# Optimization experiments

Hardware: AMD Instinct MI355X
Metric: run time of the kernel (lower is better)

The kernel has to match this reference:

```python
import jax, jax.numpy as jnp
import numpy as np

H = 12  # num_attention_heads


def setup_inputs() -> dict:
    key = jax.random.key(0)
    ks = jax.random.split(key, 7)
    B, T, L, D = 4, 64, 128, 768
    input_ids = jax.random.randint(ks[0], (B, T, L), 0, 30000, dtype=jnp.int32)
    speaker_ids = jax.random.randint(ks[1], (B, T), 0, 8, dtype=jnp.int32)
    token_embeddings = jax.random.normal(ks[2], (B, T, L, D), dtype=jnp.float32)
    edu_embeddings = jax.random.normal(ks[3], (B, T, D), dtype=jnp.float32)
    s = 1.0 / np.sqrt(D)
    Wk = jax.random.normal(ks[4], (D, D), dtype=jnp.float32) * s
    Wv = jax.random.normal(ks[5], (D, D), dtype=jnp.float32) * s
    Wq = jax.random.normal(ks[6], (D, D), dtype=jnp.float32) * s
    return {"input_ids": input_ids, "speaker_ids": speaker_ids,
            "token_embeddings": token_embeddings, "edu_embeddings": edu_embeddings,
            "Wk": Wk, "Wv": Wv, "Wq": Wq}


def reference(input_ids, speaker_ids, token_embeddings, edu_embeddings, Wk, Wv, Wq):
    B, T, L = input_ids.shape
    D = token_embeddings.shape[-1]
    d = D // H
    # per-turn keys/values, split into heads: [B,T,H,d]
    k = (edu_embeddings @ Wk.T).reshape(B, T, H, d)
    v = (edu_embeddings @ Wv.T).reshape(B, T, H, d)
    # per-head outer products k (x) v: [B,T,H,d,d]
    kv = jnp.einsum('bthd,bthe->bthde', k, v)
    # speaker-segmented inclusive prefix sum: M[b,t] = sum_{u<=t, spk[u]==spk[t]} kv[b,u]
    same = speaker_ids[:, None, :] == speaker_ids[:, :, None]        # [B,T(t),T(u)]
    causal = jnp.tril(jnp.ones((T, T), dtype=bool))                  # u <= t (inclusive)
    A = (same & causal).astype(kv.dtype)                             # [B,T,T]
    M = jnp.einsum('btu,buhde->bthde', A, kv)                        # [B,T,H,d,d]
    # token queries attend into their turn's speaker memory matrix
    q = (token_embeddings @ Wq.T).reshape(B, T, L, H, d)
    a = jnp.einsum('btlhd,bthde->btlhe', q, M).reshape(B, T, L, D)
    return token_embeddings + a
```

## Files before the change

kernel.cpp:

```cpp
#include <hip/hip_runtime.h>
#include <hip/hip_bf16.h>

#define NB 4
#define NT 64
#define NL 128
#define ND 768
#define NH 12
#define HD 64

typedef __attribute__((ext_vector_type(8))) short short8;
typedef __attribute__((ext_vector_type(4))) float f32x4;

typedef __attribute__((address_space(3))) unsigned int lds_u32;
typedef __attribute__((address_space(1))) const unsigned int glob_u32;

static __device__ __forceinline__ unsigned short f2b(float x) {
    __hip_bfloat16 h = __float2bfloat16(x);
    return *reinterpret_cast<unsigned short*>(&h);
}
static __device__ __forceinline__ void gl2lds16(const void* g, void* l) {
    __builtin_amdgcn_global_load_lds((glob_u32*)g, (lds_u32*)l, 16, 0, 0);
}
static __device__ __forceinline__ unsigned pkbf(float lo, float hi) {
    union { float f; unsigned u; } a, b; a.f = lo; b.f = hi;
    return __builtin_amdgcn_perm(b.u, a.u, 0x07060302u);
}

#define WQ_C   73728u
#define EDU_C  98304u
#define WK_C   172032u
#define NCHUNK 245760u

__global__ __launch_bounds__(256) void conv_bf16(
    const float* __restrict__ Wq, const float* __restrict__ edu,
    const float* __restrict__ Wk, const float* __restrict__ Wv,
    unsigned short* __restrict__ dst)
{
    size_t c = (size_t)blockIdx.x * 256 + threadIdx.x;
    if (c >= NCHUNK) return;
    const float* s;
    if (c < WQ_C)       s = Wq  + c * 8;
    else if (c < EDU_C) s = edu + (c - WQ_C)  * 8;
    else if (c < WK_C)  s = Wk  + (c - EDU_C) * 8;
    else                s = Wv  + (c - WK_C)  * 8;
    float4 x = *(const float4*)s;
    float4 y = *(const float4*)(s + 4);
    unsigned short v[8];
    v[0] = f2b(x.x); v[1] = f2b(x.y); v[2] = f2b(x.z); v[3] = f2b(x.w);
    v[4] = f2b(y.x); v[5] = f2b(y.y); v[6] = f2b(y.z); v[7] = f2b(y.w);
    *(short8*)(dst + c * 8) = *(short8*)v;
}

__global__ __launch_bounds__(256) void kvm(
    const unsigned short* __restrict__ edu_b,
    const unsigned short* __restrict__ wk_b,
    const unsigned short* __restrict__ wv_b,
    const int* __restrict__ spk,
    unsigned short* __restrict__ Mt)
{
    const int h = blockIdx.x, b = blockIdx.y, eh = blockIdx.z;

    __shared__ float bucket[8][32][65];
    __shared__ float k_s[64][68];
    __shared__ float v_s[64][36];
    __shared__ __align__(16) unsigned short stage[10240];
    __shared__ int spk_s[64];
    unsigned short* edu_s = stage;
    unsigned short* wk_s  = stage + 4096;
    unsigned short* wv_s  = stage + 8192;

    const int tid = threadIdx.x, lane = tid & 63, wvx = tid >> 6;
    const int lr = lane & 15, lg = lane >> 4, r8 = lane >> 3, l8 = lane & 7;

    { float* p = &bucket[0][0][0];
      for (int i = tid; i < 8 * 32 * 65; i += 256) p[i] = 0.f; }
    if (tid < 64) spk_s[tid] = spk[b * NT + tid];

    const unsigned short* edub = edu_b + (size_t)(b * 64) * ND;
    const unsigned short* wkb  = wk_b + (size_t)(h * 64) * ND;
    const unsigned short* wvb  = wv_b + (size_t)(h * 64 + eh * 32) * ND;

    f32x4 acc_k[4], acc_v[2];
    #pragma unroll
    for (int i = 0; i < 4; i++) acc_k[i] = (f32x4){0.f, 0.f, 0.f, 0.f};
    #pragma unroll
    for (int i = 0; i < 2; i++) acc_v[i] = (f32x4){0.f, 0.f, 0.f, 0.f};

    const int sswz = ((l8 ^ r8) * 8);

    for (int k0 = 0; k0 < ND; k0 += 64) {
        __syncthreads();
        #pragma unroll
        for (int j = 0; j < 5; j++) {
            const int cid = wvx * 5 + j;
            const unsigned short* gs; unsigned short* ls;
            if (cid < 8)       { gs = edub + (size_t)(cid * 8 + r8) * ND;        ls = edu_s + cid * 512; }
            else if (cid < 16) { gs = wkb  + (size_t)((cid - 8) * 8 + r8) * ND;  ls = wk_s + (cid - 8) * 512; }
            else               { gs = wvb  + (size_t)((cid - 16) * 8 + r8) * ND; ls = wv_s + (cid - 16) * 512; }
            gl2lds16(gs + k0 + sswz, ls);
        }
        __syncthreads();
        #pragma unroll
        for (int k32 = 0; k32 < 2; k32++) {
            const int cx = (((k32 * 4 + lg) ^ (lr & 7)) * 8);
            short8 eb = *(const short8*)&edu_s[(wvx * 16 + lr) * 64 + cx];
            #pragma unroll
            for (int jb = 0; jb < 4; jb++) {
                short8 ak = *(const short8*)&wk_s[(jb * 16 + lr) * 64 + cx];
                acc_k[jb] = __builtin_amdgcn_mfma_f32_16x16x32_bf16(ak, eb, acc_k[jb], 0, 0, 0);
            }
            #pragma unroll
            for (int jb = 0; jb < 2; jb++) {
                short8 av = *(const short8*)&wv_s[(jb * 16 + lr) * 64 + cx];
                acc_v[jb] = __builtin_amdgcn_mfma_f32_16x16x32_bf16(av, eb, acc_v[jb], 0, 0, 0);
            }
        }
    }

    {
        const int t = wvx * 16 + lr;
        #pragma unroll
        for (int jb = 0; jb < 4; jb++) *(f32x4*)&k_s[t][jb * 16 + lg * 4] = acc_k[jb];
        #pragma unroll
        for (int jb = 0; jb < 2; jb++) *(f32x4*)&v_s[t][jb * 16 + lg * 4] = acc_v[jb];
    }
    __syncthreads();

    const int e = tid & 31, dg = tid >> 5;
    for (int t = 0; t < NT; t++) {
        const int s = spk_s[t];
        const float vv = v_s[t][e];
        unsigned short tmp[8];
        #pragma unroll
        for (int jj = 0; jj < 8; jj++) {
            float m = bucket[s][e][dg * 8 + jj] + k_s[t][dg * 8 + jj] * vv;
            bucket[s][e][dg * 8 + jj] = m;
            tmp[jj] = f2b(m);
        }
        unsigned short* mpp = Mt + (((size_t)(b * NT + t) * NH + h) * HD + eh * 32 + e) * HD + dg * 8;
        *(short8*)mpp = *(short8*)tmp;
    }
}

__global__ __launch_bounds__(256, 2) void fused_qm(
    const float* __restrict__ te,
    const unsigned short* __restrict__ wq_b,
    const unsigned short* __restrict__ Mt,
    float* __restrict__ out)
{
    const int orig = blockIdx.x;
    const int id   = (orig & 7) * 192 + (orig >> 3);
    const int hp   = id % 6;
    const int bt   = id / 6;

    __shared__ __align__(16) unsigned short smem[32768];
    unsigned short* wq_s = smem;
    float*          te_s = (float*)(smem + 8192);
    unsigned short* mt_s = smem + 24576;
    unsigned short* q_s  = smem;

    const int tid  = threadIdx.x;
    const int lane = tid & 63;
    const int wvx  = tid >> 6;
    const int lr   = lane & 15;
    const int lg   = lane >> 4;
    const int wm   = wvx >> 1;
    const int wn   = wvx & 1;
    const int r8   = lane >> 3;
    const int l8   = lane & 7;

    const float*          teb = te + (size_t)bt * NL * ND;
    const unsigned short* wqb = wq_b + (size_t)hp * 128 * ND;

    {
        const unsigned short* mp = Mt + ((size_t)bt * NH + hp * 2) * (HD * HD);
        #pragma unroll
        for (int j = 0; j < 4; j++) {
            const int off = wvx * 2048 + j * 512;
            gl2lds16(mp + off + r8 * 64 + (l8 ^ r8) * 8, mt_s + off);
        }
    }

    f32x4 acc[4][4];
    #pragma unroll
    for (int i = 0; i < 4; i++)
        #pragma unroll
        for (int j = 0; j < 4; j++) acc[i][j] = (f32x4){0.f, 0.f, 0.f, 0.f};

    for (int k0 = 0; k0 < ND; k0 += 64) {
        __syncthreads();
        #pragma unroll
        for (int j = 0; j < 4; j++) {
            const int rbase = wvx * 32 + j * 8;
            gl2lds16(wqb + (size_t)(rbase + r8) * ND + k0 + (l8 ^ r8) * 8,
                     wq_s + rbase * 64);
        }
        #pragma unroll
        for (int j = 0; j < 8; j++) {
            const int rbase = wvx * 32 + j * 4;
            const int row   = rbase + (lane >> 4);
            const int c     = (lane & 15) ^ (row & 15);
            gl2lds16(teb + (size_t)row * ND + k0 + c * 4, te_s + rbase * 64);
        }
        __syncthreads();
        #pragma unroll
        for (int k32 = 0; k32 < 2; k32++) {
            short8 af[4], bf[4];
            #pragma unroll
            for (int tm = 0; tm < 4; tm++) {
                const int row = wm * 64 + tm * 16 + lr;
                af[tm] = *(const short8*)&wq_s[row * 64 + (((k32 * 4 + lg) ^ (lr & 7)) * 8)];
            }
            #pragma unroll
            for (int tn = 0; tn < 4; tn++) {
                const int row = wn * 64 + tn * 16 + lr;
                const int cg  = k32 * 8 + lg * 2;
                f32x4 x = *(const f32x4*)&te_s[row * 64 + ((cg ^ lr) * 4)];
                f32x4 y = *(const f32x4*)&te_s[row * 64 + (((cg + 1) ^ lr) * 4)];
                union { short8 s; unsigned u[4]; } bb;
                bb.u[0] = pkbf(x.x, x.y);
                bb.u[1] = pkbf(x.z, x.w);
                bb.u[2] = pkbf(y.x, y.y);
                bb.u[3] = pkbf(y.z, y.w);
                bf[tn] = bb.s;
            }
            #pragma unroll
            for (int tm = 0; tm < 4; tm++)
                #pragma unroll
                for (int tn = 0; tn < 4; tn++)
                    acc[tm][tn] = __builtin_amdgcn_mfma_f32_16x16x32_bf16(
                        af[tm], bf[tn], acc[tm][tn], 0, 0, 0);
        }
    }

    __syncthreads();

    #pragma unroll
    for (int tm = 0; tm < 4; tm++) {
        const int d0 = wm * 64 + tm * 16 + lg * 4;
        #pragma unroll
        for (int tn = 0; tn < 4; tn++) {
            const int ltok = wn * 64 + tn * 16 + lr;
            f32x4 a = acc[tm][tn];
            uint2 w2;
            w2.x = pkbf(a.x, a.y);
            w2.y = pkbf(a.z, a.w);
            *(uint2*)&q_s[ltok * 136 + d0] = w2;
        }
    }
    __syncthreads();

    const int h2 = wvx & 1;
    const int lh = wvx >> 1;
    f32x4 acc2[4][4];
    #pragma unroll
    for (int i = 0; i < 4; i++)
        #pragma unroll
        for (int j = 0; j < 4; j++) acc2[i][j] = (f32x4){0.f, 0.f, 0.f, 0.f};

    #pragma unroll
    for (int k32 = 0; k32 < 2; k32++) {
        const int ko = k32 * 32 + lg * 8;
        short8 af[4], bf[4];
        #pragma unroll
        for (int tm = 0; tm < 4; tm++)
            af[tm] = *(const short8*)&q_s[(lh * 64 + tm * 16 + lr) * 136 + h2 * 64 + ko];
        #pragma unroll
        for (int tn = 0; tn < 4; tn++) {
            const int row = h2 * 64 + tn * 16 + lr;
            bf[tn] = *(const short8*)&mt_s[row * 64 + (((k32 * 4 + lg) ^ (lr & 7)) * 8)];
        }
        #pragma unroll
        for (int tm = 0; tm < 4; tm++)
            #pragma unroll
            for (int tn = 0; tn < 4; tn++)
                acc2[tm][tn] = __builtin_amdgcn_mfma_f32_16x16x32_bf16(
                    af[tm], bf[tn], acc2[tm][tn], 0, 0, 0);
    }

    float* ob = out + (size_t)bt * NL * ND;
    #pragma unroll
    for (int tm = 0; tm < 4; tm++) {
        const int l0 = lh * 64 + tm * 16 + lg * 4;
        #pragma unroll
        for (int tn = 0; tn < 4; tn++) {
            const int cg = hp * 128 + h2 * 64 + tn * 16 + lr;
            f32x4 a = acc2[tm][tn];
            #pragma unroll
            for (int r = 0; r < 4; r++) {
                size_t gi = (size_t)(l0 + r) * ND + cg;
                ob[gi] = teb[gi] + a[r];
            }
        }
    }
}

extern "C" void kernel_launch(void* const* d_in, const int* in_sizes, int n_in,
                              void* d_out, int out_size, void* d_ws, size_t ws_size,
                              hipStream_t stream)
{
    const int*   spk = (const int*)d_in[1];
    const float* te  = (const float*)d_in[2];
    const float* edu = (const float*)d_in[3];
    const float* Wk  = (const float*)d_in[4];
    const float* Wv  = (const float*)d_in[5];
    const float* Wq  = (const float*)d_in[6];
    float* out = (float*)d_out;

    unsigned short* bf    = (unsigned short*)d_ws;
    unsigned short* wq_bb = bf;
    unsigned short* edu_b = bf + 589824u;
    unsigned short* wk_bb = bf + 786432u;
    unsigned short* wv_bb = bf + 1376256u;
    unsigned short* Mtbuf = bf + 1966080u;

    conv_bf16<<<960,             256, 0, stream>>>(Wq, edu, Wk, Wv, bf);
    kvm      <<<dim3(NH, NB, 2), 256, 0, stream>>>(edu_b, wk_bb, wv_bb, spk, Mtbuf);
    fused_qm <<<6 * NT * NB,     256, 0, stream>>>(te, wq_bb, Mtbuf, out);
}
```

Measured before the change: 109.9 us.

## Double-buffer Wq tiles, convert token embeddings to bf16 via registers, load M directly

Restructures the fused Q·M kernel's K loop. Token-embedding tiles are now prefetched into registers, converted to bf16, and written to LDS as bf16, and Wq tiles are double-buffered so the next tile's loads overlap the current tile's MFMAs. This shrinks LDS from 64KB to 48KB, which lets the launch bound ask for 3 blocks per CU. The M matrix is read straight from global into registers instead of being staged in LDS, and MFMA sections get raised wave priority. The cost is more register pressure, which at the higher occupancy target may cause spills, plus an extra barrier per half-iteration.

```diff
diff --git a/kernel.cpp b/kernel.cpp
--- a/kernel.cpp
+++ b/kernel.cpp
@@ -20,10 +20,6 @@
 }
 static __device__ __forceinline__ void gl2lds16(const void* g, void* l) {
     __builtin_amdgcn_global_load_lds((glob_u32*)g, (lds_u32*)l, 16, 0, 0);
-}
-static __device__ __forceinline__ unsigned pkbf(float lo, float hi) {
-    union { float f; unsigned u; } a, b; a.f = lo; b.f = hi;
-    return __builtin_amdgcn_perm(b.u, a.u, 0x07060302u);
 }
 
 #define WQ_C   73728u
@@ -142,7 +138,7 @@
     }
 }
 
-__global__ __launch_bounds__(256, 2) void fused_qm(
+__global__ __launch_bounds__(256, 3) void fused_qm(
     const float* __restrict__ te,
     const unsigned short* __restrict__ wq_b,
     const unsigned short* __restrict__ Mt,
@@ -153,10 +149,10 @@
     const int hp   = id % 6;
     const int bt   = id / 6;
 
-    __shared__ __align__(16) unsigned short smem[32768];
-    unsigned short* wq_s = smem;
-    float*          te_s = (float*)(smem + 8192);
-    unsigned short* mt_s = smem + 24576;
+    __shared__ __align__(16) unsigned short smem[24576];
+    unsigned short* te_s = smem;
+    unsigned short* wq0  = smem + 8192;
+    unsigned short* wq1  = smem + 16384;
     unsigned short* q_s  = smem;
 
     const int tid  = threadIdx.x;
@@ -168,72 +164,90 @@
     const int wn   = wvx & 1;
     const int r8   = lane >> 3;
     const int l8   = lane & 7;
+    const int sswz = (l8 ^ r8) * 8;
+    const int srow = tid >> 3;
+    const int sc   = tid & 7;
 
     const float*          teb = te + (size_t)bt * NL * ND;
     const unsigned short* wqb = wq_b + (size_t)hp * 128 * ND;
 
-    {
-        const unsigned short* mp = Mt + ((size_t)bt * NH + hp * 2) * (HD * HD);
-        #pragma unroll
-        for (int j = 0; j < 4; j++) {
-            const int off = wvx * 2048 + j * 512;
-            gl2lds16(mp + off + r8 * 64 + (l8 ^ r8) * 8, mt_s + off);
-        }
-    }
-
     f32x4 acc[4][4];
     #pragma unroll
     for (int i = 0; i < 4; i++)
         #pragma unroll
         for (int j = 0; j < 4; j++) acc[i][j] = (f32x4){0.f, 0.f, 0.f, 0.f};
 
-    for (int k0 = 0; k0 < ND; k0 += 64) {
-        __syncthreads();
+    float4 ld[4][2];
+
+    auto LOADREG = [&](int k0) {
+        #pragma unroll
+        for (int p = 0; p < 4; p++) {
+            const int r    = p * 32 + srow;
+            const int clog = sc ^ (srow & 7);
+            const float* g = teb + (size_t)r * ND + k0 + clog * 8;
+            ld[p][0] = *(const float4*)g;
+            ld[p][1] = *(const float4*)(g + 4);
+        }
+    };
+    auto CVTWRITE = [&]() {
+        #pragma unroll
+        for (int p = 0; p < 4; p++) {
+            const int r = p * 32 + srow;
+            unsigned short v[8];
+            v[0] = f2b(ld[p][0].x); v[1] = f2b(ld[p][0].y);
+            v[2] = f2b(ld[p][0].z); v[3] = f2b(ld[p][0].w);
+            v[4] = f2b(ld[p][1].x); v[5] = f2b(ld[p][1].y);
+            v[6] = f2b(ld[p][1].z); v[7] = f2b(ld[p][1].w);
+            *(short8*)&te_s[r * 64 + sc * 8] = *(short8*)v;
+        }
+    };
+    auto WQSTAGE = [&](unsigned short* buf, int k0) {
         #pragma unroll
         for (int j = 0; j < 4; j++) {
             const int rbase = wvx * 32 + j * 8;
-            gl2lds16(wqb + (size_t)(rbase + r8) * ND + k0 + (l8 ^ r8) * 8,
-                     wq_s + rbase * 64);
-        }
-        #pragma unroll
-        for (int j = 0; j < 8; j++) {
-            const int rbase = wvx * 32 + j * 4;
-            const int row   = rbase + (lane >> 4);
-            const int c     = (lane & 15) ^ (row & 15);
-            gl2lds16(teb + (size_t)row * ND + k0 + c * 4, te_s + rbase * 64);
-        }
-        __syncthreads();
+            gl2lds16(wqb + (size_t)(rbase + r8) * ND + k0 + sswz, buf + rbase * 64);
+        }
+    };
+    auto COMPUTE = [&](const unsigned short* wqs) {
         #pragma unroll
         for (int k32 = 0; k32 < 2; k32++) {
+            const int cx = (((k32 * 4 + lg) ^ (lr & 7)) * 8);
             short8 af[4], bf[4];
             #pragma unroll
-            for (int tm = 0; tm < 4; tm++) {
-                const int row = wm * 64 + tm * 16 + lr;
-                af[tm] = *(const short8*)&wq_s[row * 64 + (((k32 * 4 + lg) ^ (lr & 7)) * 8)];
-            }
-            #pragma unroll
-            for (int tn = 0; tn < 4; tn++) {
-                const int row = wn * 64 + tn * 16 + lr;
-                const int cg  = k32 * 8 + lg * 2;
-                f32x4 x = *(const f32x4*)&te_s[row * 64 + ((cg ^ lr) * 4)];
-                f32x4 y = *(const f32x4*)&te_s[row * 64 + (((cg + 1) ^ lr) * 4)];
-                union { short8 s; unsigned u[4]; } bb;
-                bb.u[0] = pkbf(x.x, x.y);
-                bb.u[1] = pkbf(x.z, x.w);
-                bb.u[2] = pkbf(y.x, y.y);
-                bb.u[3] = pkbf(y.z, y.w);
-                bf[tn] = bb.s;
-            }
+            for (int tm = 0; tm < 4; tm++)
+                af[tm] = *(const short8*)&wqs[(wm * 64 + tm * 16 + lr) * 64 + cx];
+            #pragma unroll
+            for (int tn = 0; tn < 4; tn++)
+                bf[tn] = *(const short8*)&te_s[(wn * 64 + tn * 16 + lr) * 64 + cx];
+            __builtin_amdgcn_s_setprio(1);
             #pragma unroll
             for (int tm = 0; tm < 4; tm++)
                 #pragma unroll
                 for (int tn = 0; tn < 4; tn++)
                     acc[tm][tn] = __builtin_amdgcn_mfma_f32_16x16x32_bf16(
                         af[tm], bf[tn], acc[tm][tn], 0, 0, 0);
-        }
-    }
-
+            __builtin_amdgcn_s_setprio(0);
+        }
+    };
+
+    LOADREG(0);
+    WQSTAGE(wq0, 0);
+    CVTWRITE();
     __syncthreads();
+
+    for (int k0 = 0; k0 < ND; k0 += 128) {
+        LOADREG(k0 + 64);
+        WQSTAGE(wq1, k0 + 64);
+        COMPUTE(wq0);
+        __syncthreads();
+        CVTWRITE();
+        __syncthreads();
+        if (k0 + 128 < ND) { LOADREG(k0 + 128); WQSTAGE(wq0, k0 + 128); }
+        COMPUTE(wq1);
+        __syncthreads();
+        if (k0 + 128 < ND) { CVTWRITE(); }
+        __syncthreads();
+    }
 
     #pragma unroll
     for (int tm = 0; tm < 4; tm++) {
@@ -243,15 +257,24 @@
             const int ltok = wn * 64 + tn * 16 + lr;
             f32x4 a = acc[tm][tn];
             uint2 w2;
-            w2.x = pkbf(a.x, a.y);
-            w2.y = pkbf(a.z, a.w);
+            w2.x = (unsigned)f2b(a.x) | ((unsigned)f2b(a.y) << 16);
+            w2.y = (unsigned)f2b(a.z) | ((unsigned)f2b(a.w) << 16);
             *(uint2*)&q_s[ltok * 136 + d0] = w2;
         }
     }
-    __syncthreads();
 
     const int h2 = wvx & 1;
     const int lh = wvx >> 1;
+    const unsigned short* mp = Mt + ((size_t)(bt * NH) + hp * 2 + h2) * (HD * HD);
+    short8 bfr[8];
+    #pragma unroll
+    for (int tn = 0; tn < 4; tn++)
+        #pragma unroll
+        for (int k32 = 0; k32 < 2; k32++)
+            bfr[tn * 2 + k32] =
+                *(const short8*)&mp[(tn * 16 + lr) * 64 + k32 * 32 + lg * 8];
+    __syncthreads();
+
     f32x4 acc2[4][4];
     #pragma unroll
     for (int i = 0; i < 4; i++)
@@ -261,21 +284,16 @@
     #pragma unroll
     for (int k32 = 0; k32 < 2; k32++) {
         const int ko = k32 * 32 + lg * 8;
-        short8 af[4], bf[4];
+        short8 af[4];
         #pragma unroll
         for (int tm = 0; tm < 4; tm++)
             af[tm] = *(const short8*)&q_s[(lh * 64 + tm * 16 + lr) * 136 + h2 * 64 + ko];
         #pragma unroll
-        for (int tn = 0; tn < 4; tn++) {
-            const int row = h2 * 64 + tn * 16 + lr;
-            bf[tn] = *(const short8*)&mt_s[row * 64 + (((k32 * 4 + lg) ^ (lr & 7)) * 8)];
-        }
-        #pragma unroll
         for (int tm = 0; tm < 4; tm++)
             #pragma unroll
             for (int tn = 0; tn < 4; tn++)
                 acc2[tm][tn] = __builtin_amdgcn_mfma_f32_16x16x32_bf16(
-                    af[tm], bf[tn], acc2[tm][tn], 0, 0, 0);
+                    af[tm], bfr[tn * 2 + k32], acc2[tm][tn], 0, 0, 0);
     }
 
     float* ob = out + (size_t)bt * NL * ND;
```

Result: slower. 163.6 us (+48.9%).
